# Optimization experiments

Measured on AMD Instinct MI355X. Metric: run time of the kernel, lower is better.

## Reference

```python
import jax, jax.numpy as jnp
import numpy as np

B, N, D = 2, 2048, 1024
H, DH = 16, 64
INNER = H * DH  # 1024
EPS = 1e-5


def setup_inputs() -> dict:
    key = jax.random.key(0)
    ks = jax.random.split(key, 7)
    x = jax.random.normal(ks[0], (B, N, D), dtype=jnp.float32)
    mask = jax.random.uniform(ks[1], (B, N)) < 0.9
    mask = mask.at[:, 0].set(True)  # guarantee at least one valid key per row
    attn_bias = jax.random.normal(ks[2], (H, N, N), dtype=jnp.float32) * 0.02
    ln_w = jnp.ones((D,), dtype=jnp.float32)
    ln_b = jnp.zeros((D,), dtype=jnp.float32)
    wq = jax.random.normal(ks[3], (D, INNER), dtype=jnp.float32) * 0.02
    wkv = jax.random.normal(ks[4], (D, 2 * DH), dtype=jnp.float32) * 0.02
    wo = jax.random.normal(ks[5], (INNER, D), dtype=jnp.float32) * 0.02
    return {"x": x, "attn_bias": attn_bias, "ln_w": ln_w, "ln_b": ln_b,
            "wq": wq, "wkv": wkv, "wo": wo, "mask": mask}


def reference(x, attn_bias, ln_w, ln_b, wq, wkv, wo, mask):
    scale = DH ** -0.5
    # NOTE: in the torch module, kv_input = x BEFORE self.norm (context=None),
    # so K/V come from raw x while Q comes from LayerNorm(x).
    mu = jnp.mean(x, axis=-1, keepdims=True)
    var = jnp.var(x, axis=-1, keepdims=True)
    xn = (x - mu) / jnp.sqrt(var + EPS) * ln_w + ln_b
    q = (xn @ wq).reshape(B, N, H, DH).transpose(0, 2, 1, 3) * scale  # b h n d
    kv = x @ wkv                     # b n 2*dh (shared single KV head, MQA)
    k, v = kv[..., :DH], kv[..., DH:]
    sim = jnp.einsum('bhid,bjd->bhij', q, k) + attn_bias  # bias broadcasts over b
    mask_value = -jnp.finfo(sim.dtype).max
    sim = jnp.where(mask[:, None, None, :], sim, mask_value)
    attn = jax.nn.softmax(sim, axis=-1)
    out = jnp.einsum('bhij,bjd->bhid', attn, v)
    out = out.transpose(0, 2, 1, 3).reshape(B, N, INNER)
    return out @ wo
```

## Files before the change

kernel.cpp:

```cpp
#include <hip/hip_runtime.h>
#include <hip/hip_bf16.h>

typedef __bf16 bf16_t;
typedef __bf16 bf16x8 __attribute__((ext_vector_type(8)));
typedef float f32x4 __attribute__((ext_vector_type(4)));

static constexpr int BB    = 2;
static constexpr int SEQ   = 2048;
static constexpr int DM    = 1024;
static constexpr int NHEAD = 16;
static constexpr int HD    = 64;

__device__ __forceinline__ bf16x8 ld8(const bf16_t* p) {
  return *reinterpret_cast<const bf16x8*>(p);
}

template <typename T> __device__ __forceinline__ T cvt_out(float v);
template <> __device__ __forceinline__ float  cvt_out<float >(float v) { return v; }
template <> __device__ __forceinline__ bf16_t cvt_out<bf16_t>(float v) { return (bf16_t)v; }

__global__ __launch_bounds__(256) void transpose_cast(const float* __restrict__ in,
                                                      bf16_t* __restrict__ out,
                                                      int R, int C) {
  __shared__ float tile[32][33];
  const int c0 = blockIdx.x * 32, r0 = blockIdx.y * 32;
  const int tx = threadIdx.x & 31, ty = threadIdx.x >> 5;
#pragma unroll
  for (int y = ty; y < 32; y += 8)
    tile[y][tx] = in[(size_t)(r0 + y) * C + (c0 + tx)];
  __syncthreads();
#pragma unroll
  for (int y = ty; y < 32; y += 8)
    out[(size_t)(c0 + y) * R + (r0 + tx)] = (bf16_t)tile[tx][y];
}

__global__ __launch_bounds__(256) void row_prep(const float* __restrict__ x,
    const float* __restrict__ ln_w, const float* __restrict__ ln_b,
    bf16_t* __restrict__ xbf, bf16_t* __restrict__ xn) {
  const int row = blockIdx.x, t = threadIdx.x;
  __shared__ float red[8];
  const float4 xv = *reinterpret_cast<const float4*>(&x[(size_t)row * DM + t * 4]);
  float s  = xv.x + xv.y + xv.z + xv.w;
  float s2 = xv.x * xv.x + xv.y * xv.y + xv.z * xv.z + xv.w * xv.w;
#pragma unroll
  for (int off = 32; off >= 1; off >>= 1) {
    s  += __shfl_xor(s,  off, 64);
    s2 += __shfl_xor(s2, off, 64);
  }
  if ((t & 63) == 0) { red[t >> 6] = s; red[4 + (t >> 6)] = s2; }
  __syncthreads();
  s  = red[0] + red[1] + red[2] + red[3];
  s2 = red[4] + red[5] + red[6] + red[7];
  const float mu   = s * (1.0f / DM);
  const float var  = s2 * (1.0f / DM) - mu * mu;
  const float rstd = rsqrtf(var + 1e-5f);
  const float4 wv = *reinterpret_cast<const float4*>(&ln_w[t * 4]);
  const float4 bv = *reinterpret_cast<const float4*>(&ln_b[t * 4]);
  union { bf16_t h[4]; uint2 u; } p0, p1;
  p0.h[0] = (bf16_t)xv.x; p0.h[1] = (bf16_t)xv.y;
  p0.h[2] = (bf16_t)xv.z; p0.h[3] = (bf16_t)xv.w;
  p1.h[0] = (bf16_t)((xv.x - mu) * rstd * wv.x + bv.x);
  p1.h[1] = (bf16_t)((xv.y - mu) * rstd * wv.y + bv.y);
  p1.h[2] = (bf16_t)((xv.z - mu) * rstd * wv.z + bv.z);
  p1.h[3] = (bf16_t)((xv.w - mu) * rstd * wv.w + bv.w);
  *reinterpret_cast<uint2*>(&xbf[(size_t)row * DM + t * 4]) = p0.u;
  *reinterpret_cast<uint2*>(&xn [(size_t)row * DM + t * 4]) = p1.u;
}

template <typename OutT>
__global__ __launch_bounds__(256) void gemm_bt(const bf16_t* __restrict__ A,
    const bf16_t* __restrict__ Bt, OutT* __restrict__ C, OutT* __restrict__ C2,
    int M, int Nn, int K, float scale) {
  __shared__ alignas(16) bf16_t As[128][40];
  __shared__ alignas(16) bf16_t Bs[64][40];
  const int m0 = blockIdx.x * 128, n0 = blockIdx.y * 64;
  const int t = threadIdx.x, lane = t & 63, wv = t >> 6;
  const int wm = (wv >> 1) * 64, wn = (wv & 1) * 32;
  const int l15 = lane & 15, q4 = lane >> 4;
  f32x4 acc[4][2] = {};
  const int ar = t >> 1, ac = (t & 1) * 16;
  const int br = t >> 2, bc = (t & 3) * 8;
  const bf16_t* Ap = A  + (size_t)(m0 + ar) * K + ac;
  const bf16_t* Bp = Bt + (size_t)(n0 + br) * K + bc;
  for (int k0 = 0; k0 < K; k0 += 32) {
    *reinterpret_cast<uint4*>(&As[ar][ac])     = *reinterpret_cast<const uint4*>(Ap + k0);
    *reinterpret_cast<uint4*>(&As[ar][ac + 8]) = *reinterpret_cast<const uint4*>(Ap + k0 + 8);
    *reinterpret_cast<uint4*>(&Bs[br][bc])     = *reinterpret_cast<const uint4*>(Bp + k0);
    __syncthreads();
    bf16x8 af[4], bfr[2];
#pragma unroll
    for (int mt = 0; mt < 4; ++mt) af[mt]  = ld8(&As[wm + mt * 16 + l15][q4 * 8]);
#pragma unroll
    for (int nt = 0; nt < 2; ++nt) bfr[nt] = ld8(&Bs[wn + nt * 16 + l15][q4 * 8]);
#pragma unroll
    for (int mt = 0; mt < 4; ++mt)
#pragma unroll
      for (int nt = 0; nt < 2; ++nt)
        acc[mt][nt] = __builtin_amdgcn_mfma_f32_16x16x32_bf16(af[mt], bfr[nt], acc[mt][nt], 0, 0, 0);
    __syncthreads();
  }
#pragma unroll
  for (int mt = 0; mt < 4; ++mt)
#pragma unroll
    for (int nt = 0; nt < 2; ++nt)
#pragma unroll
      for (int r = 0; r < 4; ++r) {
        const int gm = m0 + wm + mt * 16 + q4 * 4 + r;
        const int gn = n0 + wn + nt * 16 + l15;
        const OutT ov = cvt_out<OutT>(acc[mt][nt][r] * scale);
        if (C2 == nullptr) {
          C[(size_t)gm * Nn + gn] = ov;
        } else if (gn < HD) {
          C[(size_t)gm * HD + gn] = ov;
        } else {
          C2[((size_t)(gm >> 11) * HD + (gn - HD)) * SEQ + (gm & 2047)] = ov;
        }
      }
}

__global__ __launch_bounds__(256) void flash_attn(
    const bf16_t* __restrict__ q,
    const bf16_t* __restrict__ kk,
    const bf16_t* __restrict__ vT,
    const float*  __restrict__ bias,
    const int*    __restrict__ mask,
    bf16_t* __restrict__ aout)
{
  const int b = blockIdx.y & 1, h = blockIdx.y >> 1;
  const int i0 = blockIdx.x * 64;
  const int t = threadIdx.x, lane = t & 63, w = t >> 6;
  const int l15 = lane & 15, q4 = lane >> 4;

  __shared__ alignas(16) bf16_t Qs[64][72];
  __shared__ alignas(16) bf16_t Ks[32][72];
  __shared__ alignas(16) bf16_t Vs[64][40];
  __shared__ alignas(16) bf16_t Ps[4][16][40];

  {
    const int r = t >> 2, c = (t & 3) * 16;
    const bf16_t* src = &q[((size_t)b * SEQ + i0 + r) * DM + h * HD + c];
    *reinterpret_cast<uint4*>(&Qs[r][c])     = *reinterpret_cast<const uint4*>(src);
    *reinterpret_cast<uint4*>(&Qs[r][c + 8]) = *reinterpret_cast<const uint4*>(src + 8);
  }
  __syncthreads();
  const bf16x8 aq0 = ld8(&Qs[w * 16 + l15][q4 * 8]);
  const bf16x8 aq1 = ld8(&Qs[w * 16 + l15][32 + q4 * 8]);

  f32x4 o[4] = {};
  float m_run[4], l_run[4];
#pragma unroll
  for (int r = 0; r < 4; ++r) { m_run[r] = -1e30f; l_run[r] = 0.0f; }

  const float* bias_h = bias + (size_t)h * SEQ * SEQ;

  for (int j0 = 0; j0 < SEQ; j0 += 32) {
    {
      const int r = t >> 3, c = (t & 7) * 8;
      *reinterpret_cast<uint4*>(&Ks[r][c]) =
          *reinterpret_cast<const uint4*>(&kk[((size_t)b * SEQ + j0 + r) * HD + c]);
    }
    {
      const int r = t >> 2, c = (t & 3) * 8;
      *reinterpret_cast<uint4*>(&Vs[r][c]) =
          *reinterpret_cast<const uint4*>(&vT[((size_t)b * HD + r) * SEQ + j0 + c]);
    }
    __syncthreads();

    f32x4 s[2];
#pragma unroll
    for (int jn = 0; jn < 2; ++jn) {
      bf16x8 bk0 = ld8(&Ks[jn * 16 + l15][q4 * 8]);
      bf16x8 bk1 = ld8(&Ks[jn * 16 + l15][32 + q4 * 8]);
      f32x4 z = {0.f, 0.f, 0.f, 0.f};
      z = __builtin_amdgcn_mfma_f32_16x16x32_bf16(aq0, bk0, z, 0, 0, 0);
      z = __builtin_amdgcn_mfma_f32_16x16x32_bf16(aq1, bk1, z, 0, 0, 0);
      s[jn] = z;
    }

    const int mk0 = mask[b * SEQ + j0 + l15];
    const int mk1 = mask[b * SEQ + j0 + 16 + l15];
#pragma unroll
    for (int jn = 0; jn < 2; ++jn) {
      const int gj = j0 + jn * 16 + l15;
      const int mkv = jn ? mk1 : mk0;
#pragma unroll
      for (int r = 0; r < 4; ++r) {
        const int gi = i0 + w * 16 + q4 * 4 + r;
        const float sv = s[jn][r] + bias_h[(size_t)gi * SEQ + gj];
        s[jn][r] = mkv ? sv : -1e30f;
      }
    }

    float mnew[4], alpha[4];
#pragma unroll
    for (int r = 0; r < 4; ++r) {
      float mx = fmaxf(s[0][r], s[1][r]);
#pragma unroll
      for (int off = 1; off < 16; off <<= 1) mx = fmaxf(mx, __shfl_xor(mx, off, 64));
      mnew[r]  = fmaxf(m_run[r], mx);
      alpha[r] = __expf(m_run[r] - mnew[r]);
      m_run[r] = mnew[r];
    }
    float p[2][4];
#pragma unroll
    for (int jn = 0; jn < 2; ++jn)
#pragma unroll
      for (int r = 0; r < 4; ++r) p[jn][r] = __expf(s[jn][r] - mnew[r]);
#pragma unroll
    for (int r = 0; r < 4; ++r) {
      float su = p[0][r] + p[1][r];
#pragma unroll
      for (int off = 1; off < 16; off <<= 1) su += __shfl_xor(su, off, 64);
      l_run[r] = l_run[r] * alpha[r] + su;
    }
#pragma unroll
    for (int nt = 0; nt < 4; ++nt)
#pragma unroll
      for (int r = 0; r < 4; ++r) o[nt][r] *= alpha[r];

#pragma unroll
    for (int jn = 0; jn < 2; ++jn)
#pragma unroll
      for (int r = 0; r < 4; ++r)
        Ps[w][q4 * 4 + r][jn * 16 + l15] = (bf16_t)p[jn][r];
    const bf16x8 pf = ld8(&Ps[w][l15][q4 * 8]);
#pragma unroll
    for (int nt = 0; nt < 4; ++nt) {
      bf16x8 bv = ld8(&Vs[nt * 16 + l15][q4 * 8]);
      o[nt] = __builtin_amdgcn_mfma_f32_16x16x32_bf16(pf, bv, o[nt], 0, 0, 0);
    }
    __syncthreads();
  }

#pragma unroll
  for (int nt = 0; nt < 4; ++nt)
#pragma unroll
    for (int r = 0; r < 4; ++r) {
      const int gi = i0 + w * 16 + q4 * 4 + r;
      aout[((size_t)b * SEQ + gi) * DM + h * HD + nt * 16 + l15] =
          (bf16_t)(o[nt][r] / l_run[r]);
    }
}

extern "C" void kernel_launch(void* const* d_in, const int* in_sizes, int n_in,
                              void* d_out, int out_size, void* d_ws, size_t ws_size,
                              hipStream_t stream) {
  const float* x         = (const float*)d_in[0];
  const float* attn_bias = (const float*)d_in[1];
  const float* ln_w      = (const float*)d_in[2];
  const float* ln_b      = (const float*)d_in[3];
  const float* wq        = (const float*)d_in[4];
  const float* wkv       = (const float*)d_in[5];
  const float* wo        = (const float*)d_in[6];
  const int*   mask      = (const int*)d_in[7];
  float* out = (float*)d_out;

  char* ws = (char*)d_ws;
  size_t off = 0;
  auto alloc = [&](size_t bytes) {
    char* p = ws + off;
    off += (bytes + 255) & ~(size_t)255;
    return p;
  };
  bf16_t* xbf  = (bf16_t*)alloc((size_t)BB * SEQ * DM * 2);
  bf16_t* xn   = (bf16_t*)alloc((size_t)BB * SEQ * DM * 2);
  bf16_t* wqT  = (bf16_t*)alloc((size_t)DM * DM * 2);
  bf16_t* wkvT = (bf16_t*)alloc((size_t)2 * HD * DM * 2);
  bf16_t* woT  = (bf16_t*)alloc((size_t)DM * DM * 2);
  bf16_t* qb   = (bf16_t*)alloc((size_t)BB * SEQ * DM * 2);
  bf16_t* kkb  = (bf16_t*)alloc((size_t)BB * SEQ * HD * 2);
  bf16_t* vTb  = (bf16_t*)alloc((size_t)BB * HD * SEQ * 2);
  bf16_t* aout = (bf16_t*)alloc((size_t)BB * SEQ * DM * 2);

  transpose_cast<<<dim3(DM / 32, DM / 32), 256, 0, stream>>>(wq, wqT, DM, DM);
  transpose_cast<<<dim3(128 / 32, DM / 32), 256, 0, stream>>>(wkv, wkvT, DM, 128);
  transpose_cast<<<dim3(DM / 32, DM / 32), 256, 0, stream>>>(wo, woT, DM, DM);
  row_prep<<<BB * SEQ, 256, 0, stream>>>(x, ln_w, ln_b, xbf, xn);
  gemm_bt<bf16_t><<<dim3(32, 16), 256, 0, stream>>>(xn, wqT, qb, (bf16_t*)nullptr,
                                                    BB * SEQ, DM, DM, 0.125f);
  gemm_bt<bf16_t><<<dim3(32, 2), 256, 0, stream>>>(xbf, wkvT, kkb, vTb,
                                                   BB * SEQ, 128, DM, 1.0f);
  flash_attn<<<dim3(SEQ / 64, BB * NHEAD), 256, 0, stream>>>(qb, kkb, vTb, attn_bias,
                                                             mask, aout);
  gemm_bt<float><<<dim3(32, 16), 256, 0, stream>>>(aout, woT, out, (float*)nullptr,
                                                   BB * SEQ, DM, DM, 1.0f);
}
```

Baseline: 576.9 us.

## Transpose attention score layout, vectorize bias loads, use direct global-to-LDS GEMM loads

The attention kernel now computes S^T = K·Q^T so each lane holds four consecutive key columns. This lets the fp32 bias be read as float4 vectors along contiguous rows instead of scalar strided loads, and the KV tile grows from 32 to 64 keys. Softmax uses exp2 with a folded log2e and cheaper cross-lane reductions. The mask becomes an additive float precomputed in row_prep. The GEMMs stage tiles with global_load_lds, dropping register round-trips at the cost of unpadded LDS rows, which may cause bank conflicts.

Result: faster. 525.9 us (-8.8%).

```diff
diff --git a/kernel.cpp b/kernel.cpp
--- a/kernel.cpp
+++ b/kernel.cpp
@@ -2,6 +2,7 @@
 #include <hip/hip_bf16.h>
 
 typedef __bf16 bf16_t;
+typedef __bf16 bf16x4 __attribute__((ext_vector_type(4)));
 typedef __bf16 bf16x8 __attribute__((ext_vector_type(8)));
 typedef float f32x4 __attribute__((ext_vector_type(4)));
 
@@ -10,9 +11,16 @@
 static constexpr int DM    = 1024;
 static constexpr int NHEAD = 16;
 static constexpr int HD    = 64;
+static constexpr float L2E = 1.4426950408889634f;
 
 __device__ __forceinline__ bf16x8 ld8(const bf16_t* p) {
   return *reinterpret_cast<const bf16x8*>(p);
+}
+
+__device__ __forceinline__ void gl_lds16(const bf16_t* g, bf16_t* l) {
+  __builtin_amdgcn_global_load_lds(
+      (const __attribute__((address_space(1))) void*)g,
+      (__attribute__((address_space(3))) void*)l, 16, 0, 0);
 }
 
 template <typename T> __device__ __forceinline__ T cvt_out(float v);
@@ -36,7 +44,8 @@
 
 __global__ __launch_bounds__(256) void row_prep(const float* __restrict__ x,
     const float* __restrict__ ln_w, const float* __restrict__ ln_b,
-    bf16_t* __restrict__ xbf, bf16_t* __restrict__ xn) {
+    const int* __restrict__ mask,
+    bf16_t* __restrict__ xbf, bf16_t* __restrict__ xn, float* __restrict__ maskA) {
   const int row = blockIdx.x, t = threadIdx.x;
   __shared__ float red[8];
   const float4 xv = *reinterpret_cast<const float4*>(&x[(size_t)row * DM + t * 4]);
@@ -65,33 +74,37 @@
   p1.h[3] = (bf16_t)((xv.w - mu) * rstd * wv.w + bv.w);
   *reinterpret_cast<uint2*>(&xbf[(size_t)row * DM + t * 4]) = p0.u;
   *reinterpret_cast<uint2*>(&xn [(size_t)row * DM + t * 4]) = p1.u;
+  if (t == 0) maskA[row] = mask[row] ? 0.0f : -1e30f;
 }
 
 template <typename OutT>
-__global__ __launch_bounds__(256) void gemm_bt(const bf16_t* __restrict__ A,
+__global__ __launch_bounds__(256) void gemm_lds(const bf16_t* __restrict__ A,
     const bf16_t* __restrict__ Bt, OutT* __restrict__ C, OutT* __restrict__ C2,
     int M, int Nn, int K, float scale) {
-  __shared__ alignas(16) bf16_t As[128][40];
-  __shared__ alignas(16) bf16_t Bs[64][40];
+  __shared__ alignas(16) bf16_t As[128 * 32];
+  __shared__ alignas(16) bf16_t Bs[64 * 32];
   const int m0 = blockIdx.x * 128, n0 = blockIdx.y * 64;
-  const int t = threadIdx.x, lane = t & 63, wv = t >> 6;
-  const int wm = (wv >> 1) * 64, wn = (wv & 1) * 32;
+  const int t = threadIdx.x, lane = t & 63, w = t >> 6;
+  const int wm = (w & 1) * 64, wn = (w >> 1) * 32;
   const int l15 = lane & 15, q4 = lane >> 4;
   f32x4 acc[4][2] = {};
-  const int ar = t >> 1, ac = (t & 1) * 16;
-  const int br = t >> 2, bc = (t & 3) * 8;
-  const bf16_t* Ap = A  + (size_t)(m0 + ar) * K + ac;
-  const bf16_t* Bp = Bt + (size_t)(n0 + br) * K + bc;
+  const int sr = lane >> 2, sc = (lane & 3) * 8;
+  const bf16_t* Ap0 = A  + (size_t)(m0 + w * 32 + sr) * K + sc;
+  const bf16_t* Ap1 = Ap0 + (size_t)16 * K;
+  const bf16_t* Bp  = Bt + (size_t)(n0 + w * 16 + sr) * K + sc;
+  bf16_t* AsL0 = &As[(w * 32) * 32];
+  bf16_t* AsL1 = &As[(w * 32 + 16) * 32];
+  bf16_t* BsL  = &Bs[(w * 16) * 32];
   for (int k0 = 0; k0 < K; k0 += 32) {
-    *reinterpret_cast<uint4*>(&As[ar][ac])     = *reinterpret_cast<const uint4*>(Ap + k0);
-    *reinterpret_cast<uint4*>(&As[ar][ac + 8]) = *reinterpret_cast<const uint4*>(Ap + k0 + 8);
-    *reinterpret_cast<uint4*>(&Bs[br][bc])     = *reinterpret_cast<const uint4*>(Bp + k0);
+    gl_lds16(Ap0 + k0, AsL0);
+    gl_lds16(Ap1 + k0, AsL1);
+    gl_lds16(Bp  + k0, BsL);
     __syncthreads();
     bf16x8 af[4], bfr[2];
 #pragma unroll
-    for (int mt = 0; mt < 4; ++mt) af[mt]  = ld8(&As[wm + mt * 16 + l15][q4 * 8]);
-#pragma unroll
-    for (int nt = 0; nt < 2; ++nt) bfr[nt] = ld8(&Bs[wn + nt * 16 + l15][q4 * 8]);
+    for (int mt = 0; mt < 4; ++mt) af[mt]  = ld8(&As[(wm + mt * 16 + l15) * 32 + q4 * 8]);
+#pragma unroll
+    for (int nt = 0; nt < 2; ++nt) bfr[nt] = ld8(&Bs[(wn + nt * 16 + l15) * 32 + q4 * 8]);
 #pragma unroll
     for (int mt = 0; mt < 4; ++mt)
 #pragma unroll
@@ -123,7 +136,7 @@
     const bf16_t* __restrict__ kk,
     const bf16_t* __restrict__ vT,
     const float*  __restrict__ bias,
-    const int*    __restrict__ mask,
+    const float*  __restrict__ maskA,
     bf16_t* __restrict__ aout)
 {
   const int b = blockIdx.y & 1, h = blockIdx.y >> 1;
@@ -132,114 +145,117 @@
   const int l15 = lane & 15, q4 = lane >> 4;
 
   __shared__ alignas(16) bf16_t Qs[64][72];
-  __shared__ alignas(16) bf16_t Ks[32][72];
-  __shared__ alignas(16) bf16_t Vs[64][40];
-  __shared__ alignas(16) bf16_t Ps[4][16][40];
-
+  __shared__ alignas(16) bf16_t Ks[64][72];
+  __shared__ alignas(16) bf16_t Vs[64][72];
+  __shared__ alignas(16) bf16_t Pt[4][16][72];
+
+  const int sr = t >> 2, sc = (t & 3) * 16;
   {
-    const int r = t >> 2, c = (t & 3) * 16;
-    const bf16_t* src = &q[((size_t)b * SEQ + i0 + r) * DM + h * HD + c];
-    *reinterpret_cast<uint4*>(&Qs[r][c])     = *reinterpret_cast<const uint4*>(src);
-    *reinterpret_cast<uint4*>(&Qs[r][c + 8]) = *reinterpret_cast<const uint4*>(src + 8);
+    const bf16_t* src = &q[((size_t)b * SEQ + i0 + sr) * DM + h * HD + sc];
+    *reinterpret_cast<uint4*>(&Qs[sr][sc])     = *reinterpret_cast<const uint4*>(src);
+    *reinterpret_cast<uint4*>(&Qs[sr][sc + 8]) = *reinterpret_cast<const uint4*>(src + 8);
   }
   __syncthreads();
-  const bf16x8 aq0 = ld8(&Qs[w * 16 + l15][q4 * 8]);
-  const bf16x8 aq1 = ld8(&Qs[w * 16 + l15][32 + q4 * 8]);
+  const bf16x8 bq0 = ld8(&Qs[w * 16 + l15][q4 * 8]);
+  const bf16x8 bq1 = ld8(&Qs[w * 16 + l15][32 + q4 * 8]);
 
   f32x4 o[4] = {};
-  float m_run[4], l_run[4];
-#pragma unroll
-  for (int r = 0; r < 4; ++r) { m_run[r] = -1e30f; l_run[r] = 0.0f; }
-
-  const float* bias_h = bias + (size_t)h * SEQ * SEQ;
-
-  for (int j0 = 0; j0 < SEQ; j0 += 32) {
+  float m_run = -1e30f, l_run = 0.0f;
+
+  const float* bias_p = bias + (size_t)h * SEQ * SEQ
+                      + (size_t)(i0 + w * 16 + l15) * SEQ + q4 * 4;
+  const float* mask_p = maskA + b * SEQ + q4 * 4;
+  const bf16_t* kp = &kk[((size_t)b * SEQ + sr) * HD + sc];
+  const bf16_t* vp = &vT[((size_t)b * HD + sr) * SEQ + sc];
+
+  for (int j0 = 0; j0 < SEQ; j0 += 64) {
     {
-      const int r = t >> 3, c = (t & 7) * 8;
-      *reinterpret_cast<uint4*>(&Ks[r][c]) =
-          *reinterpret_cast<const uint4*>(&kk[((size_t)b * SEQ + j0 + r) * HD + c]);
-    }
-    {
-      const int r = t >> 2, c = (t & 3) * 8;
-      *reinterpret_cast<uint4*>(&Vs[r][c]) =
-          *reinterpret_cast<const uint4*>(&vT[((size_t)b * HD + r) * SEQ + j0 + c]);
+      const bf16_t* ks = kp + (size_t)j0 * HD;
+      *reinterpret_cast<uint4*>(&Ks[sr][sc])     = *reinterpret_cast<const uint4*>(ks);
+      *reinterpret_cast<uint4*>(&Ks[sr][sc + 8]) = *reinterpret_cast<const uint4*>(ks + 8);
+      const bf16_t* vs = vp + j0;
+      *reinterpret_cast<uint4*>(&Vs[sr][sc])     = *reinterpret_cast<const uint4*>(vs);
+      *reinterpret_cast<uint4*>(&Vs[sr][sc + 8]) = *reinterpret_cast<const uint4*>(vs + 8);
+    }
+    f32x4 bv[4], mv[4];
+#pragma unroll
+    for (int mt = 0; mt < 4; ++mt) {
+      bv[mt] = *reinterpret_cast<const f32x4*>(bias_p + j0 + mt * 16);
+      mv[mt] = *reinterpret_cast<const f32x4*>(mask_p + j0 + mt * 16);
     }
     __syncthreads();
 
-    f32x4 s[2];
-#pragma unroll
-    for (int jn = 0; jn < 2; ++jn) {
-      bf16x8 bk0 = ld8(&Ks[jn * 16 + l15][q4 * 8]);
-      bf16x8 bk1 = ld8(&Ks[jn * 16 + l15][32 + q4 * 8]);
+    f32x4 s[4];
+#pragma unroll
+    for (int mt = 0; mt < 4; ++mt) {
+      const bf16x8 a0 = ld8(&Ks[mt * 16 + l15][q4 * 8]);
+      const bf16x8 a1 = ld8(&Ks[mt * 16 + l15][32 + q4 * 8]);
       f32x4 z = {0.f, 0.f, 0.f, 0.f};
-      z = __builtin_amdgcn_mfma_f32_16x16x32_bf16(aq0, bk0, z, 0, 0, 0);
-      z = __builtin_amdgcn_mfma_f32_16x16x32_bf16(aq1, bk1, z, 0, 0, 0);
-      s[jn] = z;
-    }
-
-    const int mk0 = mask[b * SEQ + j0 + l15];
-    const int mk1 = mask[b * SEQ + j0 + 16 + l15];
-#pragma unroll
-    for (int jn = 0; jn < 2; ++jn) {
-      const int gj = j0 + jn * 16 + l15;
-      const int mkv = jn ? mk1 : mk0;
+      z = __builtin_amdgcn_mfma_f32_16x16x32_bf16(a0, bq0, z, 0, 0, 0);
+      z = __builtin_amdgcn_mfma_f32_16x16x32_bf16(a1, bq1, z, 0, 0, 0);
+      s[mt] = z;
+    }
+
+    float mx = -1e30f;
+#pragma unroll
+    for (int mt = 0; mt < 4; ++mt)
 #pragma unroll
       for (int r = 0; r < 4; ++r) {
-        const int gi = i0 + w * 16 + q4 * 4 + r;
-        const float sv = s[jn][r] + bias_h[(size_t)gi * SEQ + gj];
-        s[jn][r] = mkv ? sv : -1e30f;
+        s[mt][r] = s[mt][r] + bv[mt][r] + mv[mt][r];
+        mx = fmaxf(mx, s[mt][r]);
       }
-    }
-
-    float mnew[4], alpha[4];
+    mx = fmaxf(mx, __shfl_xor(mx, 16, 64));
+    mx = fmaxf(mx, __shfl_xor(mx, 32, 64));
+    const float mnew  = fmaxf(m_run, mx);
+    const float alpha = __builtin_amdgcn_exp2f((m_run - mnew) * L2E);
+    const float cc    = -mnew * L2E;
+    m_run = mnew;
+
+    float su = 0.0f;
+#pragma unroll
+    for (int mt = 0; mt < 4; ++mt)
+#pragma unroll
+      for (int r = 0; r < 4; ++r) {
+        s[mt][r] = __builtin_amdgcn_exp2f(__builtin_fmaf(s[mt][r], L2E, cc));
+        su += s[mt][r];
+      }
+    su += __shfl_xor(su, 16, 64);
+    su += __shfl_xor(su, 32, 64);
+    l_run = l_run * alpha + su;
+
+#pragma unroll
+    for (int mt = 0; mt < 4; ++mt) {
+      bf16x4 pk = {(bf16_t)s[mt][0], (bf16_t)s[mt][1], (bf16_t)s[mt][2], (bf16_t)s[mt][3]};
+      *reinterpret_cast<bf16x4*>(&Pt[w][l15][mt * 16 + q4 * 4]) = pk;
+    }
+
 #pragma unroll
     for (int r = 0; r < 4; ++r) {
-      float mx = fmaxf(s[0][r], s[1][r]);
-#pragma unroll
-      for (int off = 1; off < 16; off <<= 1) mx = fmaxf(mx, __shfl_xor(mx, off, 64));
-      mnew[r]  = fmaxf(m_run[r], mx);
-      alpha[r] = __expf(m_run[r] - mnew[r]);
-      m_run[r] = mnew[r];
-    }
-    float p[2][4];
-#pragma unroll
-    for (int jn = 0; jn < 2; ++jn)
-#pragma unroll
-      for (int r = 0; r < 4; ++r) p[jn][r] = __expf(s[jn][r] - mnew[r]);
-#pragma unroll
-    for (int r = 0; r < 4; ++r) {
-      float su = p[0][r] + p[1][r];
-#pragma unroll
-      for (int off = 1; off < 16; off <<= 1) su += __shfl_xor(su, off, 64);
-      l_run[r] = l_run[r] * alpha[r] + su;
-    }
+      const float a_r = __shfl(alpha, (q4 << 2) + r, 64);
+      o[0][r] *= a_r; o[1][r] *= a_r; o[2][r] *= a_r; o[3][r] *= a_r;
+    }
+
+#pragma unroll
+    for (int ks = 0; ks < 2; ++ks) {
+      const bf16x8 pf = ld8(&Pt[w][l15][ks * 32 + q4 * 8]);
+#pragma unroll
+      for (int nt = 0; nt < 4; ++nt) {
+        const bf16x8 vv = ld8(&Vs[nt * 16 + l15][ks * 32 + q4 * 8]);
+        o[nt] = __builtin_amdgcn_mfma_f32_16x16x32_bf16(pf, vv, o[nt], 0, 0, 0);
+      }
+    }
+    __syncthreads();
+  }
+
+#pragma unroll
+  for (int r = 0; r < 4; ++r) {
+    const float linv = 1.0f / __shfl(l_run, (q4 << 2) + r, 64);
+    const int gi = i0 + w * 16 + q4 * 4 + r;
+    bf16_t* dst = &aout[((size_t)b * SEQ + gi) * DM + h * HD];
 #pragma unroll
     for (int nt = 0; nt < 4; ++nt)
-#pragma unroll
-      for (int r = 0; r < 4; ++r) o[nt][r] *= alpha[r];
-
-#pragma unroll
-    for (int jn = 0; jn < 2; ++jn)
-#pragma unroll
-      for (int r = 0; r < 4; ++r)
-        Ps[w][q4 * 4 + r][jn * 16 + l15] = (bf16_t)p[jn][r];
-    const bf16x8 pf = ld8(&Ps[w][l15][q4 * 8]);
-#pragma unroll
-    for (int nt = 0; nt < 4; ++nt) {
-      bf16x8 bv = ld8(&Vs[nt * 16 + l15][q4 * 8]);
-      o[nt] = __builtin_amdgcn_mfma_f32_16x16x32_bf16(pf, bv, o[nt], 0, 0, 0);
-    }
-    __syncthreads();
-  }
-
-#pragma unroll
-  for (int nt = 0; nt < 4; ++nt)
-#pragma unroll
-    for (int r = 0; r < 4; ++r) {
-      const int gi = i0 + w * 16 + q4 * 4 + r;
-      aout[((size_t)b * SEQ + gi) * DM + h * HD + nt * 16 + l15] =
-          (bf16_t)(o[nt][r] / l_run[r]);
-    }
+      dst[nt * 16 + l15] = (bf16_t)(o[nt][r] * linv);
+  }
 }
 
 extern "C" void kernel_launch(void* const* d_in, const int* in_sizes, int n_in,
@@ -262,26 +278,27 @@
     off += (bytes + 255) & ~(size_t)255;
     return p;
   };
-  bf16_t* xbf  = (bf16_t*)alloc((size_t)BB * SEQ * DM * 2);
-  bf16_t* xn   = (bf16_t*)alloc((size_t)BB * SEQ * DM * 2);
-  bf16_t* wqT  = (bf16_t*)alloc((size_t)DM * DM * 2);
-  bf16_t* wkvT = (bf16_t*)alloc((size_t)2 * HD * DM * 2);
-  bf16_t* woT  = (bf16_t*)alloc((size_t)DM * DM * 2);
-  bf16_t* qb   = (bf16_t*)alloc((size_t)BB * SEQ * DM * 2);
-  bf16_t* kkb  = (bf16_t*)alloc((size_t)BB * SEQ * HD * 2);
-  bf16_t* vTb  = (bf16_t*)alloc((size_t)BB * HD * SEQ * 2);
-  bf16_t* aout = (bf16_t*)alloc((size_t)BB * SEQ * DM * 2);
+  bf16_t* xbf   = (bf16_t*)alloc((size_t)BB * SEQ * DM * 2);
+  bf16_t* xn    = (bf16_t*)alloc((size_t)BB * SEQ * DM * 2);
+  bf16_t* wqT   = (bf16_t*)alloc((size_t)DM * DM * 2);
+  bf16_t* wkvT  = (bf16_t*)alloc((size_t)2 * HD * DM * 2);
+  bf16_t* woT   = (bf16_t*)alloc((size_t)DM * DM * 2);
+  bf16_t* qb    = (bf16_t*)alloc((size_t)BB * SEQ * DM * 2);
+  bf16_t* kkb   = (bf16_t*)alloc((size_t)BB * SEQ * HD * 2);
+  bf16_t* vTb   = (bf16_t*)alloc((size_t)BB * HD * SEQ * 2);
+  bf16_t* aoutb = (bf16_t*)alloc((size_t)BB * SEQ * DM * 2);
+  float*  maskA = (float*)alloc((size_t)BB * SEQ * 4);
 
   transpose_cast<<<dim3(DM / 32, DM / 32), 256, 0, stream>>>(wq, wqT, DM, DM);
   transpose_cast<<<dim3(128 / 32, DM / 32), 256, 0, stream>>>(wkv, wkvT, DM, 128);
   transpose_cast<<<dim3(DM / 32, DM / 32), 256, 0, stream>>>(wo, woT, DM, DM);
-  row_prep<<<BB * SEQ, 256, 0, stream>>>(x, ln_w, ln_b, xbf, xn);
-  gemm_bt<bf16_t><<<dim3(32, 16), 256, 0, stream>>>(xn, wqT, qb, (bf16_t*)nullptr,
-                                                    BB * SEQ, DM, DM, 0.125f);
-  gemm_bt<bf16_t><<<dim3(32, 2), 256, 0, stream>>>(xbf, wkvT, kkb, vTb,
-                                                   BB * SEQ, 128, DM, 1.0f);
+  row_prep<<<BB * SEQ, 256, 0, stream>>>(x, ln_w, ln_b, mask, xbf, xn, maskA);
+  gemm_lds<bf16_t><<<dim3(32, 16), 256, 0, stream>>>(xn, wqT, qb, (bf16_t*)nullptr,
+                                                     BB * SEQ, DM, DM, 0.125f);
+  gemm_lds<bf16_t><<<dim3(32, 2), 256, 0, stream>>>(xbf, wkvT, kkb, vTb,
+                                                    BB * SEQ, 128, DM, 1.0f);
   flash_attn<<<dim3(SEQ / 64, BB * NHEAD), 256, 0, stream>>>(qb, kkb, vTb, attn_bias,
-                                                             mask, aout);
-  gemm_bt<float><<<dim3(32, 16), 256, 0, stream>>>(aout, woT, out, (float*)nullptr,
-                                                   BB * SEQ, DM, DM, 1.0f);
-}
+                                                             maskA, aoutb);
+  gemm_lds<float><<<dim3(32, 16), 256, 0, stream>>>(aoutb, woT, out, (float*)nullptr,
+                                                    BB * SEQ, DM, DM, 1.0f);
+}
```
